# Kernel optimization log

Measured on AMD Instinct MI355X. Metric: run time of the kernel, lower is better.

## Reference

```python
import jax, jax.numpy as jnp
import numpy as np

N_NODES = 100000
N_EDGES = 3200000

def setup_inputs() -> dict:
    key = jax.random.key(0)
    ks = jax.random.split(key, 6)
    x = jax.random.normal(ks[0], (N_NODES, 40), dtype=jnp.float32)
    src = jax.random.randint(ks[1], (N_EDGES,), 0, N_NODES, dtype=jnp.int32)
    dst = jax.random.randint(ks[2], (N_EDGES,), 0, N_NODES, dtype=jnp.int32)
    W1 = jax.random.normal(ks[3], (10, 128), dtype=jnp.float32) * 0.1
    b1 = jnp.zeros((128,), dtype=jnp.float32)
    W2 = jax.random.normal(ks[4], (128, 64), dtype=jnp.float32) * 0.1
    b2 = jnp.zeros((64,), dtype=jnp.float32)
    return {"x": x, "src": src, "dst": dst, "W1": W1, "b1": b1, "W2": W2, "b2": b2}


def reference(x, src, dst, W1, b1, W2, b2):
    N = x.shape[0]
    xs = x[:, 15:25]  # forward slices features to in_dim=10
    ones = jnp.ones(src.shape[0], dtype=x.dtype)
    deg_out = jax.ops.segment_sum(ones, src, num_segments=N)  # out-degree of src nodes
    deg_in = jax.ops.segment_sum(ones, dst, num_segments=N)   # in-degree of dst nodes
    # DGL GraphConv norm='both': clamp zero degrees to 1, symmetric 1/sqrt norm
    norm_s = jnp.where(deg_out > 0, deg_out, 1.0) ** -0.5
    norm_d = jnp.where(deg_in > 0, deg_in, 1.0) ** -0.5
    # aggregate-then-transform (in_dim < hidden_dim path in DGL)
    msgs = (xs * norm_s[:, None])[src]                         # [E, 10]
    agg = jax.ops.segment_sum(msgs, dst, num_segments=N)      # [N, 10]
    agg = agg * norm_d[:, None]
    h = agg @ W1 + b1                                          # GraphConv weight + bias
    return h @ W2 + b2                                         # linear head
```

## Files before the change

### kernel.cpp

```cpp
#include <hip/hip_runtime.h>
#include <hip/hip_fp16.h>


#define NF    10
#define COLS  40
#define OFF   15
#define H1    128
#define H2    64

#define BSH   7
#define BW    128
#define NBIN  782
#define NBINP 784
#define GS    16
#define CAPH  5632
#define PRCAP 4864
#define SENT  0xFFFFFFFFu
#define NBLKB 512
#define CHUNK 6250

#define DBLK    256
#define DCHUNKS 64
#define DRANGES 4
#define DRNG    25000
#define DRNG4   6250
#define DEDGE   50000

typedef unsigned int u32;
typedef unsigned short u16;
typedef unsigned char u8;

__device__ __forceinline__ float2 h2f(u32 u) {
    __half2 h;
    *reinterpret_cast<u32*>(&h) = u;
    return __half22float2(h);
}
__device__ __forceinline__ u32 f2h(float a, float b) {
    __half2 h = __float22half2_rn(make_float2(a, b));
    return *reinterpret_cast<u32*>(&h);
}

__global__ void __launch_bounds__(256, 4)
fusedA_kernel(const int* __restrict__ src, const int* __restrict__ dst,
              const float* __restrict__ W1, const float* __restrict__ b1,
              const float* __restrict__ W2, const float* __restrict__ b2,
              float* __restrict__ Wc, float* __restrict__ bc,
              u32* __restrict__ gcur, u32* __restrict__ srt,
              u32* __restrict__ partial32, int E, int N) {
    __shared__ union {
        struct { u32 hist[NBINP], lofs[NBINP], gbase[NBINP], lcur[NBINP], stage[CHUNK]; } pb;
        struct { u32 cnt[DRNG4]; } dg;
    } sh;
    int blk = blockIdx.x;
    int t = threadIdx.x;

    if (blk < NBLKB) {
        u32* hist = sh.pb.hist;
        u32* lofs = sh.pb.lofs;
        u32* gbase = sh.pb.gbase;
        u32* lcur = sh.pb.lcur;
        u32* stage = sh.pb.stage;
        for (int i = t; i < NBINP; i += 256) hist[i] = 0;
        __syncthreads();
        int e0 = blk * CHUNK;
        int e1 = min(E, e0 + CHUNK);
        int m = e1 - e0;

        for (int e = e0 + t; e < e1; e += 256)
            atomicAdd(&hist[dst[e] >> BSH], 1u);
        __syncthreads();

        if (t < 64) {
            u32 c[13];
            u32 seg = 0;
#pragma unroll
            for (int q = 0; q < 13; ++q) {
                int idx = t * 13 + q;
                c[q] = (idx < NBINP) ? hist[idx] : 0u;
                seg += c[q];
            }
            u32 x = seg;
#pragma unroll
            for (int off = 1; off < 64; off <<= 1) {
                u32 v = (u32)__shfl_up((int)x, off, 64);
                if (t >= off) x += v;
            }
            u32 run = x - seg;
#pragma unroll
            for (int q = 0; q < 13; ++q) {
                int idx = t * 13 + q;
                if (idx < NBINP) lofs[idx] = run;
                run += c[q];
            }
        }
        __syncthreads();

        for (int b = t; b < NBIN; b += 256) {
            u32 h = hist[b];
            u32 r = (h + 3u) & ~3u;
            gbase[b] = r ? atomicAdd(&gcur[b * GS], r) : 0u;
            lcur[b] = lofs[b];
        }
        __syncthreads();

        for (int e = e0 + t; e < e1; e += 256) {
            int d = dst[e];
            int s = src[e];
            int b = d >> BSH;
            u32 p = atomicAdd(&lcur[b], 1u);
            stage[p] = ((u32)s << BSH) | (u32)(d & (BW - 1));
        }
        __syncthreads();

        for (int i = t; i < m; i += 256) {
            u32 lo = 0, hi = NBIN;
            while (hi - lo > 1) {
                u32 mid = (lo + hi) >> 1;
                if (lofs[mid] <= (u32)i) lo = mid; else hi = mid;
            }
            u32 b = lo;
            u32 idx = gbase[b] + (u32)i - lofs[b];
            if (idx < CAPH) srt[(size_t)b * CAPH + idx] = stage[i];
        }
        for (int b = t; b < NBIN; b += 256) {
            u32 h = hist[b];
            if (!h) continue;
            u32 r = (h + 3u) & ~3u;
            for (u32 k = h; k < r; ++k) {
                u32 idx = gbase[b] + k;
                if (idx < CAPH) srt[(size_t)b * CAPH + idx] = SENT;
            }
        }
    } else if (blk < NBLKB + DBLK) {
        int idx = blk - NBLKB;
        int c = idx & (DCHUNKS - 1);
        int r = idx >> 6;
        u32* cnt = sh.dg.cnt;
        for (int i = t; i < DRNG4; i += 256) cnt[i] = 0;
        __syncthreads();
        int base = r * DRNG;
        int e0 = c * DEDGE, e1 = min(E, e0 + DEDGE);
        int nv4 = (e1 - e0) >> 2;
        const int4* s4 = (const int4*)(src + e0);
        for (int i = t; i < nv4; i += 256) {
            int4 s = s4[i];
            int a0 = s.x - base, a1 = s.y - base, a2 = s.z - base, a3 = s.w - base;
            if ((u32)a0 < (u32)DRNG) atomicAdd(&cnt[a0 >> 2], 1u << ((a0 & 3) << 3));
            if ((u32)a1 < (u32)DRNG) atomicAdd(&cnt[a1 >> 2], 1u << ((a1 & 3) << 3));
            if ((u32)a2 < (u32)DRNG) atomicAdd(&cnt[a2 >> 2], 1u << ((a2 & 3) << 3));
            if ((u32)a3 < (u32)DRNG) atomicAdd(&cnt[a3 >> 2], 1u << ((a3 & 3) << 3));
        }
        __syncthreads();
        u32* d32 = partial32 + ((size_t)c * N + base) / 4;
        for (int i = t; i < DRNG4; i += 256) d32[i] = cnt[i];
    } else {
        for (int i = t; i < NF * H2; i += 256) {
            int k = i >> 6, j = i & 63;
            float acc = 0.f;
            for (int mm = 0; mm < H1; ++mm) acc += W1[k * H1 + mm] * W2[mm * H2 + j];
            Wc[i] = acc;
        }
        for (int j = t; j < H2; j += 256) {
            float a = b2[j];
            for (int mm = 0; mm < H1; ++mm) a += b1[mm] * W2[mm * H2 + j];
            bc[j] = a;
        }
    }
}

__global__ void __launch_bounds__(256)
xsn_kernel(const float* __restrict__ x, const u8* __restrict__ partial,
           u16* __restrict__ xsn, int N) {
    int n = blockIdx.x * blockDim.x + threadIdx.x;
    if (n >= N) return;
    u32 d = 0;
#pragma unroll 4
    for (int c = 0; c < DCHUNKS; ++c) d += partial[(size_t)c * N + n];
    float norm = rsqrtf(d > 0 ? (float)d : 1.f);
    const float* xr = x + (size_t)n * COLS + OFF;
    float v[NF];
#pragma unroll
    for (int k = 0; k < NF; ++k) v[k] = xr[k] * norm;
    uint4* xo = (uint4*)(xsn + ((size_t)n << 4));
    uint4 w0, w1;
    w0.x = f2h(v[0], v[1]); w0.y = f2h(v[2], v[3]);
    w0.z = f2h(v[4], v[5]); w0.w = f2h(v[6], v[7]);
    w1.x = f2h(v[8], v[9]); w1.y = 0u; w1.z = 0u; w1.w = 0u;
    xo[0] = w0;
    xo[1] = w1;
}

__global__ void __launch_bounds__(256, 6)
passC_kernel(const u32* __restrict__ srt, const u32* __restrict__ gcur,
             const u16* __restrict__ xsn, const float* __restrict__ Wc,
             const float* __restrict__ bc, float* __restrict__ out, int N) {
    __shared__ u32 sorted[PRCAP];
    __shared__ u32 cnt[BW];
    __shared__ u32 cur[BW];
    __shared__ float sW[NF * H2];
    __shared__ float sb[H2];
    int t = threadIdx.x;
    for (int i = t; i < NF * H2; i += 256) sW[i] = Wc[i];
    if (t < H2) sb[t] = bc[t];
    if (t < BW) cnt[t] = 0;
    __syncthreads();

    int b = blockIdx.x;
    const u32* reg = srt + (size_t)b * CAPH;
    u32 m = gcur[b * GS];
    if (m > CAPH) m = CAPH;

    for (u32 e = t; e < m; e += 256) {
        u32 v = reg[e];
        if (v != SENT) atomicAdd(&cnt[v & (BW - 1)], 1u);
    }
    __syncthreads();

    if (t < 64) {
        u32 c0 = cnt[t * 2], c1 = cnt[t * 2 + 1];
        u32 seg = c0 + c1;
        u32 x = seg;
#pragma unroll
        for (int off = 1; off < 64; off <<= 1) {
            u32 v = (u32)__shfl_up((int)x, off, 64);
            if (t >= off) x += v;
        }
        u32 run = x - seg;
        cur[t * 2] = run; run += c0;
        cur[t * 2 + 1] = run;
    }
    __syncthreads();

    for (u32 e = t; e < m; e += 256) {
        u32 v = reg[e];
        if (v == SENT) continue;
        u32 p = atomicAdd(&cur[v & (BW - 1)], 1u);
        if (p < PRCAP) sorted[p] = v >> BSH;
    }
    __syncthreads();

    int node_local = t >> 2;
    int j = t & 3;
    int jb = j << 4;
#pragma unroll
    for (int sub = 0; sub < 2; ++sub) {
        int node = sub * 64 + node_local;
        u32 c   = cnt[node];
        u32 end = cur[node];
        if (end > PRCAP) end = PRCAP;
        u32 st  = (end >= c) ? end - c : 0u;
        float r0=0.f,r1=0.f,r2=0.f,r3=0.f,r4=0.f,r5=0.f,r6=0.f,r7=0.f,r8=0.f,r9=0.f;
#pragma unroll 2
        for (u32 e = st + j; e < end; e += 4) {
            const u32* xr = (const u32*)(xsn + ((size_t)sorted[e] << 4));
            uint4 p0 = *(const uint4*)xr;
            u32 p1 = xr[4];
            float2 f;
            f = h2f(p0.x); r0 += f.x; r1 += f.y;
            f = h2f(p0.y); r2 += f.x; r3 += f.y;
            f = h2f(p0.z); r4 += f.x; r5 += f.y;
            f = h2f(p0.w); r6 += f.x; r7 += f.y;
            f = h2f(p1);   r8 += f.x; r9 += f.y;
        }
#define QRED(r) r += __shfl_xor(r, 1, 64); r += __shfl_xor(r, 2, 64)
        QRED(r0); QRED(r1); QRED(r2); QRED(r3); QRED(r4);
        QRED(r5); QRED(r6); QRED(r7); QRED(r8); QRED(r9);
#undef QRED
        int n = (b << BSH) + node;
        if (n < N) {
            float norm = rsqrtf(c > 0 ? (float)c : 1.f);
            r0 *= norm; r1 *= norm; r2 *= norm; r3 *= norm; r4 *= norm;
            r5 *= norm; r6 *= norm; r7 *= norm; r8 *= norm; r9 *= norm;
            float o[16];
#pragma unroll
            for (int q = 0; q < 16; ++q) o[q] = sb[jb + q];
            float rr[NF] = {r0,r1,r2,r3,r4,r5,r6,r7,r8,r9};
#pragma unroll
            for (int k = 0; k < NF; ++k) {
                float a = rr[k];
#pragma unroll
                for (int q = 0; q < 16; ++q) o[q] += a * sW[k * H2 + jb + q];
            }
            float* op = out + (size_t)n * H2 + jb;
            *(float4*)(op)      = make_float4(o[0], o[1], o[2], o[3]);
            *(float4*)(op + 4)  = make_float4(o[4], o[5], o[6], o[7]);
            *(float4*)(op + 8)  = make_float4(o[8], o[9], o[10], o[11]);
            *(float4*)(op + 12) = make_float4(o[12], o[13], o[14], o[15]);
        }
    }
}

extern "C" void kernel_launch(void* const* d_in, const int* in_sizes, int n_in,
                              void* d_out, int out_size, void* d_ws, size_t ws_size,
                              hipStream_t stream) {
    const float* x   = (const float*)d_in[0];
    const int*   src = (const int*)d_in[1];
    const int*   dst = (const int*)d_in[2];
    const float* W1  = (const float*)d_in[3];
    const float* b1  = (const float*)d_in[4];
    const float* W2  = (const float*)d_in[5];
    const float* b2  = (const float*)d_in[6];
    float* out = (float*)d_out;

    const int N = in_sizes[0] / COLS;
    const int E = in_sizes[1];

    float* ws = (float*)d_ws;
    float* Wc   = ws;
    float* bc   = Wc + NF * H2;
    u32*   gcur = (u32*)(bc + H2);
    size_t off_u32 = (size_t)(NF * H2 + H2) + (size_t)NBIN * GS;
    off_u32 = (off_u32 + 15) & ~(size_t)15;
    u16*   xsn = (u16*)((u32*)d_ws + off_u32);
    u32*   srt = (u32*)d_ws + off_u32 + (size_t)N * 8;
    u32*   partial32 = srt + (size_t)NBIN * CAPH;
    const u8* partial8 = (const u8*)partial32;

    hipMemsetAsync(gcur, 0, (size_t)NBIN * GS * sizeof(u32), stream);

    fusedA_kernel<<<NBLKB + DBLK + 1, 256, 0, stream>>>(
        src, dst, W1, b1, W2, b2, Wc, bc, gcur, srt, partial32, E, N);

    xsn_kernel<<<(N + 255) / 256, 256, 0, stream>>>(x, partial8, xsn, N);

    passC_kernel<<<NBIN, 256, 0, stream>>>(srt, gcur, xsn, Wc, bc, out, N);
}
```

Baseline: 205.0 us.

## Fuse all phases into one persistent kernel with grid-wide barriers

Merges the binning/degree pass, the normalized-feature conversion and the aggregation/projection pass into one kernel launched with one block per bin, separated by atomic-counter grid barriers. This removes two kernel launches and their inter-kernel gaps. It also resizes the edge chunk per block so that 782 blocks cover all edges. The change relies on all 782 blocks being co-resident, with a deadlock risk if they are not. It hardcodes the edge counts per degree chunk (no E bounds check) and raises shared-memory use with the union.

```diff
diff --git a/kernel.cpp b/kernel.cpp
--- a/kernel.cpp
+++ b/kernel.cpp
@@ -16,8 +16,7 @@
 #define CAPH  5632
 #define PRCAP 4864
 #define SENT  0xFFFFFFFFu
-#define NBLKB 512
-#define CHUNK 6250
+#define CHUNK 4096
 
 #define DBLK    256
 #define DCHUNKS 64
@@ -40,21 +39,39 @@
     return *reinterpret_cast<u32*>(&h);
 }
 
+__device__ __forceinline__ void grid_barrier(u32* ctr, u32 nblk) {
+    __syncthreads();
+    if (threadIdx.x == 0) {
+        __threadfence();
+        u32 arrived = atomicAdd(ctr, 1u) + 1;
+        if (arrived < nblk) {
+            while (__hip_atomic_load(ctr, __ATOMIC_ACQUIRE, __HIP_MEMORY_SCOPE_AGENT) < nblk)
+                __builtin_amdgcn_s_sleep(2);
+        }
+        __threadfence();
+    }
+    __syncthreads();
+}
+
 __global__ void __launch_bounds__(256, 4)
-fusedA_kernel(const int* __restrict__ src, const int* __restrict__ dst,
-              const float* __restrict__ W1, const float* __restrict__ b1,
-              const float* __restrict__ W2, const float* __restrict__ b2,
-              float* __restrict__ Wc, float* __restrict__ bc,
-              u32* __restrict__ gcur, u32* __restrict__ srt,
-              u32* __restrict__ partial32, int E, int N) {
+gcn_kernel(const float* __restrict__ x,
+           const int* __restrict__ src, const int* __restrict__ dst,
+           const float* __restrict__ W1, const float* __restrict__ b1,
+           const float* __restrict__ W2, const float* __restrict__ b2,
+           float* __restrict__ Wc, float* __restrict__ bc,
+           u32* __restrict__ gcur, u32* __restrict__ bar,
+           u16* __restrict__ xsn, u32* __restrict__ srt,
+           u32* __restrict__ partial32, float* __restrict__ out,
+           int E, int N) {
     __shared__ union {
         struct { u32 hist[NBINP], lofs[NBINP], gbase[NBINP], lcur[NBINP], stage[CHUNK]; } pb;
         struct { u32 cnt[DRNG4]; } dg;
+        struct { u32 sorted[PRCAP], cnt[BW], cur[BW]; float sW[NF * H2], sb[H2]; } pc;
     } sh;
     int blk = blockIdx.x;
     int t = threadIdx.x;
 
-    if (blk < NBLKB) {
+    {
         u32* hist = sh.pb.hist;
         u32* lofs = sh.pb.lofs;
         u32* gbase = sh.pb.gbase;
@@ -79,13 +96,13 @@
                 c[q] = (idx < NBINP) ? hist[idx] : 0u;
                 seg += c[q];
             }
-            u32 x = seg;
+            u32 xx = seg;
 #pragma unroll
             for (int off = 1; off < 64; off <<= 1) {
-                u32 v = (u32)__shfl_up((int)x, off, 64);
-                if (t >= off) x += v;
-            }
-            u32 run = x - seg;
+                u32 v = (u32)__shfl_up((int)xx, off, 64);
+                if (t >= off) xx += v;
+            }
+            u32 run = xx - seg;
 #pragma unroll
             for (int q = 0; q < 13; ++q) {
                 int idx = t * 13 + q;
@@ -131,16 +148,18 @@
                 if (idx < CAPH) srt[(size_t)b * CAPH + idx] = SENT;
             }
         }
-    } else if (blk < NBLKB + DBLK) {
-        int idx = blk - NBLKB;
-        int c = idx & (DCHUNKS - 1);
-        int r = idx >> 6;
+    }
+    __syncthreads();
+
+    if (blk < DBLK) {
+        int c = blk & (DCHUNKS - 1);
+        int r = blk >> 6;
         u32* cnt = sh.dg.cnt;
         for (int i = t; i < DRNG4; i += 256) cnt[i] = 0;
         __syncthreads();
         int base = r * DRNG;
-        int e0 = c * DEDGE, e1 = min(E, e0 + DEDGE);
-        int nv4 = (e1 - e0) >> 2;
+        int e0 = c * DEDGE;
+        int nv4 = DEDGE >> 2;
         const int4* s4 = (const int4*)(src + e0);
         for (int i = t; i < nv4; i += 256) {
             int4 s = s4[i];
@@ -153,7 +172,7 @@
         __syncthreads();
         u32* d32 = partial32 + ((size_t)c * N + base) / 4;
         for (int i = t; i < DRNG4; i += 256) d32[i] = cnt[i];
-    } else {
+    } else if (blk == NBIN - 1) {
         for (int i = t; i < NF * H2; i += 256) {
             int k = i >> 6, j = i & 63;
             float acc = 0.f;
@@ -166,126 +185,126 @@
             bc[j] = a;
         }
     }
-}
-
-__global__ void __launch_bounds__(256)
-xsn_kernel(const float* __restrict__ x, const u8* __restrict__ partial,
-           u16* __restrict__ xsn, int N) {
-    int n = blockIdx.x * blockDim.x + threadIdx.x;
-    if (n >= N) return;
-    u32 d = 0;
+
+    grid_barrier(bar, NBIN);
+
+    {
+        int n = blk * 256 + t;
+        if (n < N) {
+            u32 d = 0;
+            const u8* partial8 = (const u8*)partial32;
 #pragma unroll 4
-    for (int c = 0; c < DCHUNKS; ++c) d += partial[(size_t)c * N + n];
-    float norm = rsqrtf(d > 0 ? (float)d : 1.f);
-    const float* xr = x + (size_t)n * COLS + OFF;
-    float v[NF];
-#pragma unroll
-    for (int k = 0; k < NF; ++k) v[k] = xr[k] * norm;
-    uint4* xo = (uint4*)(xsn + ((size_t)n << 4));
-    uint4 w0, w1;
-    w0.x = f2h(v[0], v[1]); w0.y = f2h(v[2], v[3]);
-    w0.z = f2h(v[4], v[5]); w0.w = f2h(v[6], v[7]);
-    w1.x = f2h(v[8], v[9]); w1.y = 0u; w1.z = 0u; w1.w = 0u;
-    xo[0] = w0;
-    xo[1] = w1;
-}
-
-__global__ void __launch_bounds__(256, 6)
-passC_kernel(const u32* __restrict__ srt, const u32* __restrict__ gcur,
-             const u16* __restrict__ xsn, const float* __restrict__ Wc,
-             const float* __restrict__ bc, float* __restrict__ out, int N) {
-    __shared__ u32 sorted[PRCAP];
-    __shared__ u32 cnt[BW];
-    __shared__ u32 cur[BW];
-    __shared__ float sW[NF * H2];
-    __shared__ float sb[H2];
-    int t = threadIdx.x;
-    for (int i = t; i < NF * H2; i += 256) sW[i] = Wc[i];
-    if (t < H2) sb[t] = bc[t];
-    if (t < BW) cnt[t] = 0;
-    __syncthreads();
-
-    int b = blockIdx.x;
-    const u32* reg = srt + (size_t)b * CAPH;
-    u32 m = gcur[b * GS];
-    if (m > CAPH) m = CAPH;
-
-    for (u32 e = t; e < m; e += 256) {
-        u32 v = reg[e];
-        if (v != SENT) atomicAdd(&cnt[v & (BW - 1)], 1u);
-    }
-    __syncthreads();
-
-    if (t < 64) {
-        u32 c0 = cnt[t * 2], c1 = cnt[t * 2 + 1];
-        u32 seg = c0 + c1;
-        u32 x = seg;
-#pragma unroll
-        for (int off = 1; off < 64; off <<= 1) {
-            u32 v = (u32)__shfl_up((int)x, off, 64);
-            if (t >= off) x += v;
-        }
-        u32 run = x - seg;
-        cur[t * 2] = run; run += c0;
-        cur[t * 2 + 1] = run;
-    }
-    __syncthreads();
-
-    for (u32 e = t; e < m; e += 256) {
-        u32 v = reg[e];
-        if (v == SENT) continue;
-        u32 p = atomicAdd(&cur[v & (BW - 1)], 1u);
-        if (p < PRCAP) sorted[p] = v >> BSH;
-    }
-    __syncthreads();
-
-    int node_local = t >> 2;
-    int j = t & 3;
-    int jb = j << 4;
-#pragma unroll
-    for (int sub = 0; sub < 2; ++sub) {
-        int node = sub * 64 + node_local;
-        u32 c   = cnt[node];
-        u32 end = cur[node];
-        if (end > PRCAP) end = PRCAP;
-        u32 st  = (end >= c) ? end - c : 0u;
-        float r0=0.f,r1=0.f,r2=0.f,r3=0.f,r4=0.f,r5=0.f,r6=0.f,r7=0.f,r8=0.f,r9=0.f;
+            for (int c = 0; c < DCHUNKS; ++c) d += partial8[(size_t)c * N + n];
+            float norm = rsqrtf(d > 0 ? (float)d : 1.f);
+            const float* xr = x + (size_t)n * COLS + OFF;
+            float v[NF];
+#pragma unroll
+            for (int k = 0; k < NF; ++k) v[k] = xr[k] * norm;
+            uint4* xo = (uint4*)(xsn + ((size_t)n << 4));
+            uint4 w0, w1;
+            w0.x = f2h(v[0], v[1]); w0.y = f2h(v[2], v[3]);
+            w0.z = f2h(v[4], v[5]); w0.w = f2h(v[6], v[7]);
+            w1.x = f2h(v[8], v[9]); w1.y = 0u; w1.z = 0u; w1.w = 0u;
+            xo[0] = w0;
+            xo[1] = w1;
+        }
+    }
+
+    grid_barrier(bar + GS, NBIN);
+
+    {
+        u32* sorted = sh.pc.sorted;
+        u32* cnt = sh.pc.cnt;
+        u32* cur = sh.pc.cur;
+        float* sW = sh.pc.sW;
+        float* sb = sh.pc.sb;
+        for (int i = t; i < NF * H2; i += 256) sW[i] = Wc[i];
+        if (t < H2) sb[t] = bc[t];
+        if (t < BW) cnt[t] = 0;
+        __syncthreads();
+
+        int b = blk;
+        const u32* reg = srt + (size_t)b * CAPH;
+        u32 m = gcur[b * GS];
+        if (m > CAPH) m = CAPH;
+
+        for (u32 e = t; e < m; e += 256) {
+            u32 v = reg[e];
+            if (v != SENT) atomicAdd(&cnt[v & (BW - 1)], 1u);
+        }
+        __syncthreads();
+
+        if (t < 64) {
+            u32 c0 = cnt[t * 2], c1 = cnt[t * 2 + 1];
+            u32 seg = c0 + c1;
+            u32 xx = seg;
+#pragma unroll
+            for (int off = 1; off < 64; off <<= 1) {
+                u32 v = (u32)__shfl_up((int)xx, off, 64);
+                if (t >= off) xx += v;
+            }
+            u32 run = xx - seg;
+            cur[t * 2] = run; run += c0;
+            cur[t * 2 + 1] = run;
+        }
+        __syncthreads();
+
+        for (u32 e = t; e < m; e += 256) {
+            u32 v = reg[e];
+            if (v == SENT) continue;
+            u32 p = atomicAdd(&cur[v & (BW - 1)], 1u);
+            if (p < PRCAP) sorted[p] = v >> BSH;
+        }
+        __syncthreads();
+
+        int node_local = t >> 2;
+        int j = t & 3;
+        int jb = j << 4;
+#pragma unroll
+        for (int sub = 0; sub < 2; ++sub) {
+            int node = sub * 64 + node_local;
+            u32 c   = cnt[node];
+            u32 end = cur[node];
+            if (end > PRCAP) end = PRCAP;
+            u32 st  = (end >= c) ? end - c : 0u;
+            float r0=0.f,r1=0.f,r2=0.f,r3=0.f,r4=0.f,r5=0.f,r6=0.f,r7=0.f,r8=0.f,r9=0.f;
 #pragma unroll 2
-        for (u32 e = st + j; e < end; e += 4) {
-            const u32* xr = (const u32*)(xsn + ((size_t)sorted[e] << 4));
-            uint4 p0 = *(const uint4*)xr;
-            u32 p1 = xr[4];
-            float2 f;
-            f = h2f(p0.x); r0 += f.x; r1 += f.y;
-            f = h2f(p0.y); r2 += f.x; r3 += f.y;
-            f = h2f(p0.z); r4 += f.x; r5 += f.y;
-            f = h2f(p0.w); r6 += f.x; r7 += f.y;
-            f = h2f(p1);   r8 += f.x; r9 += f.y;
-        }
+            for (u32 e = st + j; e < end; e += 4) {
+                const u32* xr = (const u32*)(xsn + ((size_t)sorted[e] << 4));
+                uint4 p0 = *(const uint4*)xr;
+                u32 p1 = xr[4];
+                float2 f;
+                f = h2f(p0.x); r0 += f.x; r1 += f.y;
+                f = h2f(p0.y); r2 += f.x; r3 += f.y;
+                f = h2f(p0.z); r4 += f.x; r5 += f.y;
+                f = h2f(p0.w); r6 += f.x; r7 += f.y;
+                f = h2f(p1);   r8 += f.x; r9 += f.y;
+            }
 #define QRED(r) r += __shfl_xor(r, 1, 64); r += __shfl_xor(r, 2, 64)
-        QRED(r0); QRED(r1); QRED(r2); QRED(r3); QRED(r4);
-        QRED(r5); QRED(r6); QRED(r7); QRED(r8); QRED(r9);
+            QRED(r0); QRED(r1); QRED(r2); QRED(r3); QRED(r4);
+            QRED(r5); QRED(r6); QRED(r7); QRED(r8); QRED(r9);
 #undef QRED
-        int n = (b << BSH) + node;
-        if (n < N) {
-            float norm = rsqrtf(c > 0 ? (float)c : 1.f);
-            r0 *= norm; r1 *= norm; r2 *= norm; r3 *= norm; r4 *= norm;
-            r5 *= norm; r6 *= norm; r7 *= norm; r8 *= norm; r9 *= norm;
-            float o[16];
-#pragma unroll
-            for (int q = 0; q < 16; ++q) o[q] = sb[jb + q];
-            float rr[NF] = {r0,r1,r2,r3,r4,r5,r6,r7,r8,r9};
-#pragma unroll
-            for (int k = 0; k < NF; ++k) {
-                float a = rr[k];
-#pragma unroll
-                for (int q = 0; q < 16; ++q) o[q] += a * sW[k * H2 + jb + q];
-            }
-            float* op = out + (size_t)n * H2 + jb;
-            *(float4*)(op)      = make_float4(o[0], o[1], o[2], o[3]);
-            *(float4*)(op + 4)  = make_float4(o[4], o[5], o[6], o[7]);
-            *(float4*)(op + 8)  = make_float4(o[8], o[9], o[10], o[11]);
-            *(float4*)(op + 12) = make_float4(o[12], o[13], o[14], o[15]);
+            int n = (b << BSH) + node;
+            if (n < N) {
+                float norm = rsqrtf(c > 0 ? (float)c : 1.f);
+                r0 *= norm; r1 *= norm; r2 *= norm; r3 *= norm; r4 *= norm;
+                r5 *= norm; r6 *= norm; r7 *= norm; r8 *= norm; r9 *= norm;
+                float o[16];
+#pragma unroll
+                for (int q = 0; q < 16; ++q) o[q] = sb[jb + q];
+                float rr[NF] = {r0,r1,r2,r3,r4,r5,r6,r7,r8,r9};
+#pragma unroll
+                for (int k = 0; k < NF; ++k) {
+                    float a = rr[k];
+#pragma unroll
+                    for (int q = 0; q < 16; ++q) o[q] += a * sW[k * H2 + jb + q];
+                }
+                float* op = out + (size_t)n * H2 + jb;
+                *(float4*)(op)      = make_float4(o[0], o[1], o[2], o[3]);
+                *(float4*)(op + 4)  = make_float4(o[4], o[5], o[6], o[7]);
+                *(float4*)(op + 8)  = make_float4(o[8], o[9], o[10], o[11]);
+                *(float4*)(op + 12) = make_float4(o[12], o[13], o[14], o[15]);
+            }
         }
     }
 }
@@ -309,19 +328,15 @@
     float* Wc   = ws;
     float* bc   = Wc + NF * H2;
     u32*   gcur = (u32*)(bc + H2);
-    size_t off_u32 = (size_t)(NF * H2 + H2) + (size_t)NBIN * GS;
-    off_u32 = (off_u32 + 15) & ~(size_t)15;
-    u16*   xsn = (u16*)((u32*)d_ws + off_u32);
-    u32*   srt = (u32*)d_ws + off_u32 + (size_t)N * 8;
+    u32*   bar  = gcur + (size_t)NBIN * GS;
+    u32*   xsn32 = bar + 32;
+    u16*   xsn  = (u16*)xsn32;
+    u32*   srt  = xsn32 + (size_t)N * 8;
     u32*   partial32 = srt + (size_t)NBIN * CAPH;
-    const u8* partial8 = (const u8*)partial32;
-
-    hipMemsetAsync(gcur, 0, (size_t)NBIN * GS * sizeof(u32), stream);
-
-    fusedA_kernel<<<NBLKB + DBLK + 1, 256, 0, stream>>>(
-        src, dst, W1, b1, W2, b2, Wc, bc, gcur, srt, partial32, E, N);
-
-    xsn_kernel<<<(N + 255) / 256, 256, 0, stream>>>(x, partial8, xsn, N);
-
-    passC_kernel<<<NBIN, 256, 0, stream>>>(srt, gcur, xsn, Wc, bc, out, N);
-}
+
+    hipMemsetAsync(gcur, 0, ((size_t)NBIN * GS + 32) * sizeof(u32), stream);
+
+    gcn_kernel<<<NBIN, 256, 0, stream>>>(x, src, dst, W1, b1, W2, b2,
+                                         Wc, bc, gcur, bar, xsn, srt,
+                                         partial32, out, E, N);
+}
```

Measured after the change: 755.2 us. +268.3%, slower.

## Drop sentinel padding, rebalance binning chunks, parallelize degree reduction in xsn

Applied to the files above, without the earlier changes.

The binning pass now uses one block per 4096-edge chunk (782 blocks) instead of 512 blocks of 6250 edges, and launch bounds move from 4 to 5 blocks per SM. Bin slots are no longer padded to multiples of four, so the sentinel fill loop and the sentinel checks in the aggregation kernel go away, and the per-bin capacity shrinks. The xsn kernel now splits each node's 64-chunk degree sum across four lanes and combines them with shuffles, to hide more load latency per node. The degree blocks now assume a fixed edge count per chunk, and any bin larger than the smaller capacity would silently drop edges.

```diff
diff --git a/kernel.cpp b/kernel.cpp
--- a/kernel.cpp
+++ b/kernel.cpp
@@ -13,11 +13,9 @@
 #define NBIN  782
 #define NBINP 784
 #define GS    16
-#define CAPH  5632
+#define CAPH  4864
 #define PRCAP 4864
-#define SENT  0xFFFFFFFFu
-#define NBLKB 512
-#define CHUNK 6250
+#define CHUNK 4096
 
 #define DBLK    256
 #define DCHUNKS 64
@@ -40,7 +38,7 @@
     return *reinterpret_cast<u32*>(&h);
 }
 
-__global__ void __launch_bounds__(256, 4)
+__global__ void __launch_bounds__(256, 5)
 fusedA_kernel(const int* __restrict__ src, const int* __restrict__ dst,
               const float* __restrict__ W1, const float* __restrict__ b1,
               const float* __restrict__ W2, const float* __restrict__ b2,
@@ -54,7 +52,7 @@
     int blk = blockIdx.x;
     int t = threadIdx.x;
 
-    if (blk < NBLKB) {
+    if (blk < NBIN) {
         u32* hist = sh.pb.hist;
         u32* lofs = sh.pb.lofs;
         u32* gbase = sh.pb.gbase;
@@ -79,13 +77,13 @@
                 c[q] = (idx < NBINP) ? hist[idx] : 0u;
                 seg += c[q];
             }
-            u32 x = seg;
+            u32 xx = seg;
 #pragma unroll
             for (int off = 1; off < 64; off <<= 1) {
-                u32 v = (u32)__shfl_up((int)x, off, 64);
-                if (t >= off) x += v;
-            }
-            u32 run = x - seg;
+                u32 v = (u32)__shfl_up((int)xx, off, 64);
+                if (t >= off) xx += v;
+            }
+            u32 run = xx - seg;
 #pragma unroll
             for (int q = 0; q < 13; ++q) {
                 int idx = t * 13 + q;
@@ -97,8 +95,7 @@
 
         for (int b = t; b < NBIN; b += 256) {
             u32 h = hist[b];
-            u32 r = (h + 3u) & ~3u;
-            gbase[b] = r ? atomicAdd(&gcur[b * GS], r) : 0u;
+            gbase[b] = h ? atomicAdd(&gcur[b * GS], h) : 0u;
             lcur[b] = lofs[b];
         }
         __syncthreads();
@@ -122,25 +119,16 @@
             u32 idx = gbase[b] + (u32)i - lofs[b];
             if (idx < CAPH) srt[(size_t)b * CAPH + idx] = stage[i];
         }
-        for (int b = t; b < NBIN; b += 256) {
-            u32 h = hist[b];
-            if (!h) continue;
-            u32 r = (h + 3u) & ~3u;
-            for (u32 k = h; k < r; ++k) {
-                u32 idx = gbase[b] + k;
-                if (idx < CAPH) srt[(size_t)b * CAPH + idx] = SENT;
-            }
-        }
-    } else if (blk < NBLKB + DBLK) {
-        int idx = blk - NBLKB;
+    } else if (blk < NBIN + DBLK) {
+        int idx = blk - NBIN;
         int c = idx & (DCHUNKS - 1);
         int r = idx >> 6;
         u32* cnt = sh.dg.cnt;
         for (int i = t; i < DRNG4; i += 256) cnt[i] = 0;
         __syncthreads();
         int base = r * DRNG;
-        int e0 = c * DEDGE, e1 = min(E, e0 + DEDGE);
-        int nv4 = (e1 - e0) >> 2;
+        int e0 = c * DEDGE;
+        int nv4 = DEDGE >> 2;
         const int4* s4 = (const int4*)(src + e0);
         for (int i = t; i < nv4; i += 256) {
             int4 s = s4[i];
@@ -171,23 +159,30 @@
 __global__ void __launch_bounds__(256)
 xsn_kernel(const float* __restrict__ x, const u8* __restrict__ partial,
            u16* __restrict__ xsn, int N) {
-    int n = blockIdx.x * blockDim.x + threadIdx.x;
+    int t = threadIdx.x;
+    int n = blockIdx.x * 64 + (t >> 2);
+    int j = t & 3;
     if (n >= N) return;
     u32 d = 0;
-#pragma unroll 4
-    for (int c = 0; c < DCHUNKS; ++c) d += partial[(size_t)c * N + n];
-    float norm = rsqrtf(d > 0 ? (float)d : 1.f);
-    const float* xr = x + (size_t)n * COLS + OFF;
-    float v[NF];
-#pragma unroll
-    for (int k = 0; k < NF; ++k) v[k] = xr[k] * norm;
-    uint4* xo = (uint4*)(xsn + ((size_t)n << 4));
-    uint4 w0, w1;
-    w0.x = f2h(v[0], v[1]); w0.y = f2h(v[2], v[3]);
-    w0.z = f2h(v[4], v[5]); w0.w = f2h(v[6], v[7]);
-    w1.x = f2h(v[8], v[9]); w1.y = 0u; w1.z = 0u; w1.w = 0u;
-    xo[0] = w0;
-    xo[1] = w1;
+#pragma unroll
+    for (int q = 0; q < 16; ++q)
+        d += partial[(size_t)(j * 16 + q) * N + n];
+    d += __shfl_xor((int)d, 1, 64);
+    d += __shfl_xor((int)d, 2, 64);
+    if (j == 0) {
+        float norm = rsqrtf(d > 0 ? (float)d : 1.f);
+        const float* xr = x + (size_t)n * COLS + OFF;
+        float v[NF];
+#pragma unroll
+        for (int k = 0; k < NF; ++k) v[k] = xr[k] * norm;
+        uint4* xo = (uint4*)(xsn + ((size_t)n << 4));
+        uint4 w0, w1;
+        w0.x = f2h(v[0], v[1]); w0.y = f2h(v[2], v[3]);
+        w0.z = f2h(v[4], v[5]); w0.w = f2h(v[6], v[7]);
+        w1.x = f2h(v[8], v[9]); w1.y = 0u; w1.z = 0u; w1.w = 0u;
+        xo[0] = w0;
+        xo[1] = w1;
+    }
 }
 
 __global__ void __launch_bounds__(256, 6)
@@ -210,22 +205,20 @@
     u32 m = gcur[b * GS];
     if (m > CAPH) m = CAPH;
 
-    for (u32 e = t; e < m; e += 256) {
-        u32 v = reg[e];
-        if (v != SENT) atomicAdd(&cnt[v & (BW - 1)], 1u);
-    }
+    for (u32 e = t; e < m; e += 256)
+        atomicAdd(&cnt[reg[e] & (BW - 1)], 1u);
     __syncthreads();
 
     if (t < 64) {
         u32 c0 = cnt[t * 2], c1 = cnt[t * 2 + 1];
         u32 seg = c0 + c1;
-        u32 x = seg;
+        u32 xx = seg;
 #pragma unroll
         for (int off = 1; off < 64; off <<= 1) {
-            u32 v = (u32)__shfl_up((int)x, off, 64);
-            if (t >= off) x += v;
-        }
-        u32 run = x - seg;
+            u32 v = (u32)__shfl_up((int)xx, off, 64);
+            if (t >= off) xx += v;
+        }
+        u32 run = xx - seg;
         cur[t * 2] = run; run += c0;
         cur[t * 2 + 1] = run;
     }
@@ -233,7 +226,6 @@
 
     for (u32 e = t; e < m; e += 256) {
         u32 v = reg[e];
-        if (v == SENT) continue;
         u32 p = atomicAdd(&cur[v & (BW - 1)], 1u);
         if (p < PRCAP) sorted[p] = v >> BSH;
     }
@@ -309,19 +301,18 @@
     float* Wc   = ws;
     float* bc   = Wc + NF * H2;
     u32*   gcur = (u32*)(bc + H2);
-    size_t off_u32 = (size_t)(NF * H2 + H2) + (size_t)NBIN * GS;
-    off_u32 = (off_u32 + 15) & ~(size_t)15;
-    u16*   xsn = (u16*)((u32*)d_ws + off_u32);
-    u32*   srt = (u32*)d_ws + off_u32 + (size_t)N * 8;
+    u32*   xsn32 = gcur + (size_t)NBIN * GS;
+    u16*   xsn  = (u16*)xsn32;
+    u32*   srt  = xsn32 + (size_t)N * 8;
     u32*   partial32 = srt + (size_t)NBIN * CAPH;
     const u8* partial8 = (const u8*)partial32;
 
     hipMemsetAsync(gcur, 0, (size_t)NBIN * GS * sizeof(u32), stream);
 
-    fusedA_kernel<<<NBLKB + DBLK + 1, 256, 0, stream>>>(
+    fusedA_kernel<<<NBIN + DBLK + 1, 256, 0, stream>>>(
         src, dst, W1, b1, W2, b2, Wc, bc, gcur, srt, partial32, E, N);
 
-    xsn_kernel<<<(N + 255) / 256, 256, 0, stream>>>(x, partial8, xsn, N);
+    xsn_kernel<<<(N + 63) / 64, 256, 0, stream>>>(x, partial8, xsn, N);
 
     passC_kernel<<<NBIN, 256, 0, stream>>>(srt, gcur, xsn, Wc, bc, out, N);
 }
```

Result: slower. 212.0 us (+3.4%).
